# Kernel tuning notes

Hardware: AMD Instinct MI355X
Metric: run time of the kernel (lower is better)

## Reference

```python
import jax, jax.numpy as jnp
import numpy as np


def setup_inputs() -> dict:
    key = jax.random.key(0)
    k1, k2, k3 = jax.random.split(key, 3)
    B, T, C = 16, 8192, 128  # batch, tokens, max_columns
    column_logits = jax.random.normal(k1, (B, T, C), dtype=jnp.float32)
    column_assignments = jax.random.randint(k2, (B, T), 0, C)
    valid_mask = jax.random.randint(k3, (B, T), 0, 2).astype(bool)
    return {
        "column_logits": column_logits,
        "column_assignments": column_assignments,
        "valid_mask": valid_mask,
    }


def reference(column_logits, column_assignments, valid_mask):
    # column_logits: (B, T, C); column_assignments: (B, T) int; valid_mask: (B, T) bool
    B, T, C = column_logits.shape
    probs = jax.nn.softmax(column_logits, axis=-1).reshape(-1, C)  # (N, C)
    seg = column_assignments.reshape(-1)                           # (N,)
    w = valid_mask.reshape(-1).astype(probs.dtype)                 # (N,)

    # Single-pass segmented stats over column ids (num_segments = max_columns).
    n = jax.ops.segment_sum(w, seg, num_segments=C)                       # (C,)
    s = jax.ops.segment_sum(probs * w[:, None], seg, num_segments=C)      # (C, C)
    n_safe = jnp.maximum(n, 1.0)
    mean = s / n_safe[:, None]                                            # per-column mean prob

    # Sum of squared deviations (matches torch's ((p - mean)**2).mean()).
    diff = probs - mean[seg]
    ssd = jax.ops.segment_sum((diff * diff) * w[:, None], seg, num_segments=C)  # (C, C)
    col_var = ssd.sum(axis=-1) / (n_safe * C)                                    # (C,)

    has_multi = n > 1.0  # columns with at least 2 valid tokens
    count = has_multi.sum().astype(col_var.dtype)
    total = jnp.where(has_multi, col_var, 0.0).sum()
    return jnp.where(count > 0, total / jnp.maximum(count, 1.0), 0.0)
```

## Files before the change

kernel.cpp:

```cpp
#include <hip/hip_runtime.h>
#include <hip/hip_bf16.h>


#define NROWS 131072
#define CC    128
#define NB    256
#define RPB   512

typedef float f32x16 __attribute__((ext_vector_type(16)));
typedef short bf16x8 __attribute__((ext_vector_type(8)));

union U4V { uint4 u; bf16x8 v; };
union H2U { __hip_bfloat162 h; unsigned int u; };

__global__ __launch_bounds__(1024) void fused_kernel(
    const float* __restrict__ logits, const int* __restrict__ seg,
    const int* __restrict__ mask, float* __restrict__ slab_s,
    float* __restrict__ slab_n, float* __restrict__ slab_q) {
  __shared__ ushort Plds[RPB * CC];
  __shared__ int sm[RPB];
  __shared__ unsigned int sg4[128];
  __shared__ float n_lds[CC], q_lds[CC];
  const int t = threadIdx.x, b = blockIdx.x;
  if (t < CC) { n_lds[t] = 0.f; q_lds[t] = 0.f; }
  if (t < RPB) {
    const int r = b * RPB + t;
    sm[t] = seg[r] | (mask[r] << 16);
  }
  __syncthreads();
  if (t < 128) {
    unsigned int w = 0;
#pragma unroll
    for (int k = 0; k < 4; ++k) {
      const int smv = sm[t * 4 + k];
      const unsigned int sv = (smv >> 16) ? (unsigned int)(smv & 0xFFFF) : 255u;
      w |= sv << (8 * k);
    }
    sg4[t] = w;
  }

  const int wave = t >> 6, lane = t & 63;
  const int q = lane >> 5, j5 = lane & 31;
#pragma unroll
  for (int g = 0; g < 2; ++g) {
    const int ts = 2 * wave + g;
    const int rb = ts * 16 + q * 8;
    float x[8][4];
#pragma unroll
    for (int i = 0; i < 8; ++i) {
      const float* rp = logits + (size_t)(b * RPB + rb + i) * CC + j5;
#pragma unroll
      for (int nt = 0; nt < 4; ++nt) x[i][nt] = rp[nt * 32];
    }
    float inv[8], qr[8];
#pragma unroll
    for (int i = 0; i < 8; ++i) {
      float z = 0.f, z2 = 0.f;
#pragma unroll
      for (int nt = 0; nt < 4; ++nt) {
        const float e = __expf(x[i][nt]);
        x[i][nt] = e; z += e; z2 += e * e;
      }
#pragma unroll
      for (int off = 1; off < 32; off <<= 1) {
        z  += __shfl_xor(z, off, 64);
        z2 += __shfl_xor(z2, off, 64);
      }
      inv[i] = 1.0f / z;
      qr[i] = z2 * inv[i] * inv[i];
    }
#pragma unroll
    for (int nt = 0; nt < 4; ++nt) {
      unsigned int d[4];
#pragma unroll
      for (int k = 0; k < 4; ++k) {
        H2U h;
        h.h = __float22bfloat162_rn(make_float2(
            x[2 * k][nt] * inv[2 * k], x[2 * k + 1][nt] * inv[2 * k + 1]));
        d[k] = h.u;
      }
      *(uint4*)(Plds + ((size_t)(ts * 4 + nt) * 64 + lane) * 8) =
          make_uint4(d[0], d[1], d[2], d[3]);
    }
    if (j5 == 0) {
#pragma unroll
      for (int i = 0; i < 8; ++i) {
        const int smv = sm[rb + i];
        if (smv >> 16) {
          atomicAdd(&n_lds[smv & 0xFFFF], 1.0f);
          atomicAdd(&q_lds[smv & 0xFFFF], qr[i]);
        }
      }
    }
  }
  __syncthreads();

  if (t >= 256 && t < 384) slab_n[(t - 256) * NB + b] = n_lds[t - 256];
  else if (t >= 384 && t < 512) slab_q[(t - 384) * NB + b] = q_lds[t - 384];

  if (wave < 4) {
    const int mm = wave * 32 + (lane & 31);
    f32x16 acc0 = {}, acc1 = {}, acc2 = {}, acc3 = {};
    const ushort* pl = Plds + (size_t)lane * 8;
    for (int ks = 0; ks < 32; ++ks) {
      const unsigned int w0 = sg4[ks * 4 + q * 2];
      const unsigned int w1 = sg4[ks * 4 + q * 2 + 1];
      U4V a;
      {
        const unsigned int s0 = w0 & 255u, s1 = (w0 >> 8) & 255u;
        const unsigned int s2 = (w0 >> 16) & 255u, s3 = w0 >> 24;
        const unsigned int s4 = w1 & 255u, s5 = (w1 >> 8) & 255u;
        const unsigned int s6 = (w1 >> 16) & 255u, s7 = w1 >> 24;
        const unsigned int um = (unsigned int)mm;
        a.u = make_uint4(
            (s0 == um ? 0x3F80u : 0u) | (s1 == um ? 0x3F800000u : 0u),
            (s2 == um ? 0x3F80u : 0u) | (s3 == um ? 0x3F800000u : 0u),
            (s4 == um ? 0x3F80u : 0u) | (s5 == um ? 0x3F800000u : 0u),
            (s6 == um ? 0x3F80u : 0u) | (s7 == um ? 0x3F800000u : 0u));
      }
      U4V b0, b1, b2, b3;
      b0.u = *(const uint4*)(pl + (size_t)(ks * 4 + 0) * 512);
      b1.u = *(const uint4*)(pl + (size_t)(ks * 4 + 1) * 512);
      b2.u = *(const uint4*)(pl + (size_t)(ks * 4 + 2) * 512);
      b3.u = *(const uint4*)(pl + (size_t)(ks * 4 + 3) * 512);
      acc0 = __builtin_amdgcn_mfma_f32_32x32x16_bf16(a.v, b0.v, acc0, 0, 0, 0);
      acc1 = __builtin_amdgcn_mfma_f32_32x32x16_bf16(a.v, b1.v, acc1, 0, 0, 0);
      acc2 = __builtin_amdgcn_mfma_f32_32x32x16_bf16(a.v, b2.v, acc2, 0, 0, 0);
      acc3 = __builtin_amdgcn_mfma_f32_32x32x16_bf16(a.v, b3.v, acc3, 0, 0, 0);
    }
    float* outp = slab_s + (size_t)b * (CC * CC);
    const int jcol = lane & 31;
    const int rbase = (lane >> 5) * 4;
#pragma unroll
    for (int reg = 0; reg < 16; ++reg) {
      const int c = wave * 32 + (reg & 3) + 8 * (reg >> 2) + rbase;
      outp[c * CC + 0 * 32 + jcol] = acc0[reg];
      outp[c * CC + 1 * 32 + jcol] = acc1[reg];
      outp[c * CC + 2 * 32 + jcol] = acc2[reg];
      outp[c * CC + 3 * 32 + jcol] = acc3[reg];
    }
  }
}

__global__ __launch_bounds__(1024) void k3_colvar(
    const float* __restrict__ slab_s, const float* __restrict__ slab_n,
    const float* __restrict__ slab_q, float* __restrict__ colvar,
    float* __restrict__ flag) {
  const int c = blockIdx.x, t = threadIdx.x;
  const int j = t & 127, g8 = t >> 7;
  const float* base = slab_s + (size_t)g8 * (CC * CC) + (size_t)c * CC + j;
  float acc = 0.f;
#pragma unroll
  for (int i = 0; i < 32; ++i) acc += base[(size_t)(8 * i) * (CC * CC)];
  __shared__ float part[8 * CC];
  part[g8 * CC + j] = acc;
  __syncthreads();
  float tp = 0.f, np = 0.f, qp = 0.f;
  if (t < CC) {
    float s = 0.f;
#pragma unroll
    for (int g = 0; g < 8; ++g) s += part[g * CC + t];
    tp = s * s;
  } else if (t < 2 * CC) {
    const int k = t - CC;
    np = slab_n[c * NB + k] + slab_n[c * NB + k + 128];
  } else if (t < 3 * CC) {
    const int k = t - 2 * CC;
    qp = slab_q[c * NB + k] + slab_q[c * NB + k + 128];
  }
#pragma unroll
  for (int off = 32; off > 0; off >>= 1) {
    tp += __shfl_xor(tp, off, 64);
    np += __shfl_xor(np, off, 64);
    qp += __shfl_xor(qp, off, 64);
  }
  __shared__ float fin[3 * 16];
  if ((t & 63) == 0) {
    const int w = t >> 6;
    fin[w * 3 + 0] = tp; fin[w * 3 + 1] = np; fin[w * 3 + 2] = qp;
  }
  __syncthreads();
  if (t == 0) {
    float tt = 0.f, nn = 0.f, qq = 0.f;
#pragma unroll
    for (int i = 0; i < 16; ++i) {
      tt += fin[i * 3 + 0]; nn += fin[i * 3 + 1]; qq += fin[i * 3 + 2];
    }
    float cv = 0.f, fl = 0.f;
    if (nn > 1.0f) {
      cv = (qq - tt / nn) / (nn * (float)CC);
      fl = 1.f;
    }
    colvar[c] = cv;
    flag[c] = fl;
  }
}

__global__ __launch_bounds__(128) void final_k(
    const float* __restrict__ colvar, const float* __restrict__ flag,
    float* __restrict__ out) {
  const int j = threadIdx.x;
  float cv = colvar[j];
  float fl = flag[j];
#pragma unroll
  for (int off = 32; off > 0; off >>= 1) {
    cv += __shfl_xor(cv, off, 64);
    fl += __shfl_xor(fl, off, 64);
  }
  __shared__ float red[4];
  if ((j & 63) == 0) {
    const int w = j >> 6;
    red[w * 2 + 0] = cv;
    red[w * 2 + 1] = fl;
  }
  __syncthreads();
  if (j == 0) {
    const float total = red[0] + red[2];
    const float count = red[1] + red[3];
    out[0] = (count > 0.f) ? total / fmaxf(count, 1.f) : 0.f;
  }
}

extern "C" void kernel_launch(void* const* d_in, const int* in_sizes, int n_in,
                              void* d_out, int out_size, void* d_ws,
                              size_t ws_size, hipStream_t stream) {
  const float* logits = (const float*)d_in[0];
  const int* seg = (const int*)d_in[1];
  const int* mask = (const int*)d_in[2];
  float* out = (float*)d_out;

  float* slab_s = (float*)d_ws;
  float* slab_n = slab_s + (size_t)NB * CC * CC;
  float* slab_q = slab_n + CC * NB;
  float* colvar = slab_q + CC * NB;
  float* flag = colvar + CC;
  fused_kernel<<<NB, 1024, 0, stream>>>(logits, seg, mask, slab_s, slab_n,
                                        slab_q);
  k3_colvar<<<CC, 1024, 0, stream>>>(slab_s, slab_n, slab_q, colvar, flag);
  final_k<<<1, 128, 0, stream>>>(colvar, flag, out);
}
```

Before: 109.0 us.

## Vectorize logits loads and slab stores, fold final reduction into colvar via ticket

Each lane now loads a contiguous float4 of logits per row instead of four strided scalars. Accumulator slabs are written as float4 using a permuted column order, which stays consistent because k3 sums squares over all columns. The separate final kernel is removed: colvar blocks atomically accumulate into scalars, and the last block, found with a ticket counter, writes the output. This saves one launch and some memory transactions, at the cost of atomic ordering and non-deterministic float summation.

```diff
diff --git a/kernel.cpp b/kernel.cpp
--- a/kernel.cpp
+++ b/kernel.cpp
@@ -16,12 +16,16 @@
 __global__ __launch_bounds__(1024) void fused_kernel(
     const float* __restrict__ logits, const int* __restrict__ seg,
     const int* __restrict__ mask, float* __restrict__ slab_s,
-    float* __restrict__ slab_n, float* __restrict__ slab_q) {
+    float* __restrict__ slab_n, float* __restrict__ slab_q,
+    float* __restrict__ scal, unsigned int* __restrict__ ticket) {
   __shared__ ushort Plds[RPB * CC];
   __shared__ int sm[RPB];
   __shared__ unsigned int sg4[128];
   __shared__ float n_lds[CC], q_lds[CC];
   const int t = threadIdx.x, b = blockIdx.x;
+  if (b == 0 && t == 1023) {
+    scal[0] = 0.f; scal[1] = 0.f; *ticket = 0u;
+  }
   if (t < CC) { n_lds[t] = 0.f; q_lds[t] = 0.f; }
   if (t < RPB) {
     const int r = b * RPB + t;
@@ -45,22 +49,19 @@
   for (int g = 0; g < 2; ++g) {
     const int ts = 2 * wave + g;
     const int rb = ts * 16 + q * 8;
-    float x[8][4];
+    float4 x[8];
+#pragma unroll
+    for (int i = 0; i < 8; ++i)
+      x[i] = ((const float4*)(logits + (size_t)(b * RPB + rb + i) * CC))[j5];
+    float inv[8], qr[8];
 #pragma unroll
     for (int i = 0; i < 8; ++i) {
-      const float* rp = logits + (size_t)(b * RPB + rb + i) * CC + j5;
-#pragma unroll
-      for (int nt = 0; nt < 4; ++nt) x[i][nt] = rp[nt * 32];
-    }
-    float inv[8], qr[8];
-#pragma unroll
-    for (int i = 0; i < 8; ++i) {
-      float z = 0.f, z2 = 0.f;
-#pragma unroll
-      for (int nt = 0; nt < 4; ++nt) {
-        const float e = __expf(x[i][nt]);
-        x[i][nt] = e; z += e; z2 += e * e;
-      }
+      float4 e;
+      e.x = __expf(x[i].x); e.y = __expf(x[i].y);
+      e.z = __expf(x[i].z); e.w = __expf(x[i].w);
+      x[i] = e;
+      float z = (e.x + e.y) + (e.z + e.w);
+      float z2 = (e.x * e.x + e.y * e.y) + (e.z * e.z + e.w * e.w);
 #pragma unroll
       for (int off = 1; off < 32; off <<= 1) {
         z  += __shfl_xor(z, off, 64);
@@ -74,9 +75,11 @@
       unsigned int d[4];
 #pragma unroll
       for (int k = 0; k < 4; ++k) {
+        const float* xa = (const float*)&x[2 * k];
+        const float* xb = (const float*)&x[2 * k + 1];
         H2U h;
-        h.h = __float22bfloat162_rn(make_float2(
-            x[2 * k][nt] * inv[2 * k], x[2 * k + 1][nt] * inv[2 * k + 1]));
+        h.h = __float22bfloat162_rn(
+            make_float2(xa[nt] * inv[2 * k], xb[nt] * inv[2 * k + 1]));
         d[k] = h.u;
       }
       *(uint4*)(Plds + ((size_t)(ts * 4 + nt) * 64 + lane) * 8) =
@@ -134,18 +137,16 @@
 #pragma unroll
     for (int reg = 0; reg < 16; ++reg) {
       const int c = wave * 32 + (reg & 3) + 8 * (reg >> 2) + rbase;
-      outp[c * CC + 0 * 32 + jcol] = acc0[reg];
-      outp[c * CC + 1 * 32 + jcol] = acc1[reg];
-      outp[c * CC + 2 * 32 + jcol] = acc2[reg];
-      outp[c * CC + 3 * 32 + jcol] = acc3[reg];
+      *(float4*)(outp + c * CC + 4 * jcol) =
+          make_float4(acc0[reg], acc1[reg], acc2[reg], acc3[reg]);
     }
   }
 }
 
 __global__ __launch_bounds__(1024) void k3_colvar(
     const float* __restrict__ slab_s, const float* __restrict__ slab_n,
-    const float* __restrict__ slab_q, float* __restrict__ colvar,
-    float* __restrict__ flag) {
+    const float* __restrict__ slab_q, float* __restrict__ scal,
+    unsigned int* __restrict__ ticket, float* __restrict__ out) {
   const int c = blockIdx.x, t = threadIdx.x;
   const int j = t & 127, g8 = t >> 7;
   const float* base = slab_s + (size_t)g8 * (CC * CC) + (size_t)c * CC + j;
@@ -191,33 +192,15 @@
       cv = (qq - tt / nn) / (nn * (float)CC);
       fl = 1.f;
     }
-    colvar[c] = cv;
-    flag[c] = fl;
-  }
-}
-
-__global__ __launch_bounds__(128) void final_k(
-    const float* __restrict__ colvar, const float* __restrict__ flag,
-    float* __restrict__ out) {
-  const int j = threadIdx.x;
-  float cv = colvar[j];
-  float fl = flag[j];
-#pragma unroll
-  for (int off = 32; off > 0; off >>= 1) {
-    cv += __shfl_xor(cv, off, 64);
-    fl += __shfl_xor(fl, off, 64);
-  }
-  __shared__ float red[4];
-  if ((j & 63) == 0) {
-    const int w = j >> 6;
-    red[w * 2 + 0] = cv;
-    red[w * 2 + 1] = fl;
-  }
-  __syncthreads();
-  if (j == 0) {
-    const float total = red[0] + red[2];
-    const float count = red[1] + red[3];
-    out[0] = (count > 0.f) ? total / fmaxf(count, 1.f) : 0.f;
+    atomicAdd(&scal[0], cv);
+    atomicAdd(&scal[1], fl);
+    __threadfence();
+    const unsigned int old = atomicAdd(ticket, 1u);
+    if (old == CC - 1) {
+      const float total = atomicAdd(&scal[0], 0.f);
+      const float count = atomicAdd(&scal[1], 0.f);
+      out[0] = (count > 0.f) ? total / fmaxf(count, 1.f) : 0.f;
+    }
   }
 }
 
@@ -232,10 +215,10 @@
   float* slab_s = (float*)d_ws;
   float* slab_n = slab_s + (size_t)NB * CC * CC;
   float* slab_q = slab_n + CC * NB;
-  float* colvar = slab_q + CC * NB;
-  float* flag = colvar + CC;
+  float* scal = slab_q + CC * NB;
+  unsigned int* ticket = (unsigned int*)(scal + 2);
   fused_kernel<<<NB, 1024, 0, stream>>>(logits, seg, mask, slab_s, slab_n,
-                                        slab_q);
-  k3_colvar<<<CC, 1024, 0, stream>>>(slab_s, slab_n, slab_q, colvar, flag);
-  final_k<<<1, 128, 0, stream>>>(colvar, flag, out);
+                                        slab_q, scal, ticket);
+  k3_colvar<<<CC, 1024, 0, stream>>>(slab_s, slab_n, slab_q, scal, ticket,
+                                     out);
 }
```

Result: slower. 112.9 us (+3.6%).
